# Performance work log

Hardware: AMD Instinct MI355X
Metric: run time of the kernel (lower is better)

Reference implementation:

```python
import jax, jax.numpy as jnp
import numpy as np
import math

B, NPG, DEG = 100, 500, 12          # graphs, nodes/graph, avg degree
F_IN, H, C = 128, 128, 10
RATIO = 0.5
N = B * NPG
E = N * DEG
K1 = math.ceil(NPG * RATIO)          # 250
K2 = math.ceil(K1 * RATIO)           # 125
K3 = math.ceil(K2 * RATIO)           # 63


def _lin(k, i, o):
    return jax.random.uniform(k, (i, o), jnp.float32, -1.0, 1.0) / np.sqrt(i).astype(np.float32)


def setup_inputs() -> dict:
    key = jax.random.key(0)
    ks = jax.random.split(key, 16)
    x = jax.random.normal(ks[0], (N, F_IN), jnp.float32)
    off = (jnp.arange(B, dtype=jnp.int32) * NPG)[:, None]
    src = (jax.random.randint(ks[1], (B, NPG * DEG), 0, NPG, jnp.int32) + off).reshape(-1)
    dst = (jax.random.randint(ks[2], (B, NPG * DEG), 0, NPG, jnp.int32) + off).reshape(-1)
    edge_index = jnp.stack([src, dst])
    return {
        'x': x, 'edge_index': edge_index,
        'Wl1': _lin(ks[3], F_IN, H), 'bl1': jnp.zeros((H,), jnp.float32), 'Wr1': _lin(ks[4], F_IN, H),
        'Wl2': _lin(ks[5], H, H), 'bl2': jnp.zeros((H,), jnp.float32), 'Wr2': _lin(ks[6], H, H),
        'Wl3': _lin(ks[7], H, H), 'bl3': jnp.zeros((H,), jnp.float32), 'Wr3': _lin(ks[8], H, H),
        'pw1': jax.random.normal(ks[9], (H,), jnp.float32),
        'pw2': jax.random.normal(ks[10], (H,), jnp.float32),
        'pw3': jax.random.normal(ks[11], (H,), jnp.float32),
        'W1': _lin(ks[12], 2 * H, H), 'b1': jnp.zeros((H,), jnp.float32),
        'W2': _lin(ks[13], H, H // 2), 'b2': jnp.zeros((H // 2,), jnp.float32),
        'W3': _lin(ks[14], H // 2, C), 'b3': jnp.zeros((C,), jnp.float32),
    }


def sage_conv(x, src, dst, emask, Wl, bl, Wr, n_nodes):
    # PyG SAGEConv: out_i = lin_l(mean_{j->i} x_j) + lin_r(x_i)
    msg = x[src] * emask[:, None]                                   # [E, d]
    agg = jax.ops.segment_sum(msg, dst, num_segments=n_nodes)
    cnt = jax.ops.segment_sum(emask, dst, num_segments=n_nodes)
    mean = agg / jnp.maximum(cnt, 1.0)[:, None]
    return mean @ Wl + bl + x @ Wr


def topk_pool(x, w, src, dst, emask, n_per, k):
    # TopKPooling: score = tanh(x.w/||w||); keep top-k nodes per graph; x_kept *= score
    score = jnp.tanh((x @ w) / jnp.linalg.norm(w))                  # [B*n_per]
    topv, topi = jax.lax.top_k(score.reshape(B, n_per), k)          # [B, k]
    perm = (topi + (jnp.arange(B, dtype=jnp.int32) * n_per)[:, None]).reshape(-1)
    x_new = x[perm] * topv.reshape(-1)[:, None]                     # [B*k, d]
    mapping = jnp.full((B * n_per,), -1, jnp.int32).at[perm].set(jnp.arange(B * k, dtype=jnp.int32))
    ns, nd = mapping[src], mapping[dst]
    emask_new = emask * ((ns >= 0) & (nd >= 0)).astype(emask.dtype)
    return x_new, jnp.maximum(ns, 0), jnp.maximum(nd, 0), emask_new


def readout(x, k):
    # global_max_pool || global_mean_pool (all graphs have exactly k nodes)
    xr = x.reshape(B, k, H)
    return jnp.concatenate([xr.max(axis=1), xr.mean(axis=1)], axis=1)  # [B, 2H]


def reference(x, edge_index, Wl1, bl1, Wr1, Wl2, bl2, Wr2, Wl3, bl3, Wr3,
              pw1, pw2, pw3, W1, b1, W2, b2, W3, b3):
    src, dst = edge_index[0], edge_index[1]
    emask = jnp.ones((E,), jnp.float32)
    h = jax.nn.relu(sage_conv(x, src, dst, emask, Wl1, bl1, Wr1, N))
    h, src, dst, emask = topk_pool(h, pw1, src, dst, emask, NPG, K1)
    x1 = readout(h, K1)
    h = jax.nn.relu(sage_conv(h, src, dst, emask, Wl2, bl2, Wr2, B * K1))
    h, src, dst, emask = topk_pool(h, pw2, src, dst, emask, K1, K2)
    x2 = readout(h, K2)
    h = jax.nn.relu(sage_conv(h, src, dst, emask, Wl3, bl3, Wr3, B * K2))
    h, src, dst, emask = topk_pool(h, pw3, src, dst, emask, K2, K3)
    x3 = readout(h, K3)
    z = x1 + x2 + x3
    z = jax.nn.relu(z @ W1 + b1)   # dropout is identity in eval mode
    z = jax.nn.relu(z @ W2 + b2)
    return jax.nn.log_softmax(z @ W3 + b3, axis=1)   # pool_loss == 0 for TopKPool
```

## Files before the change

### kernel.cpp

```cpp
#include <hip/hip_runtime.h>
#include <math.h>

#define BG    100
#define NPG   500
#define FD    128
#define EE    600000
#define EPG   6000
#define NN    50000
#define K1    250
#define K2    125
#define K3    63
#define CAP   64

typedef short v8s __attribute__((ext_vector_type(8)));
typedef float v4f __attribute__((ext_vector_type(4)));

__device__ __forceinline__ int swz(int p, int N) {
    int j = p & 7, i = p >> 3;
    int chunk = N >> 3, rem = N & 7;
    int mj = j < rem ? j : rem;
    return j * chunk + mj + i;
}

__device__ __forceinline__ unsigned short f2bf(float f) {
    unsigned int u = __float_as_uint(f);
    unsigned int r = (u + 0x7FFFu + ((u >> 16) & 1u)) >> 16;
    return (unsigned short)r;
}
__device__ __forceinline__ float bf2f(unsigned short b) {
    return __uint_as_float(((unsigned int)b) << 16);
}

__global__ __launch_bounds__(1024) void prep_fill_kernel(
        const int* __restrict__ ei, int* __restrict__ deg, int* __restrict__ col,
        const float* __restrict__ Wl1, const float* __restrict__ Wr1,
        const float* __restrict__ Wl2, const float* __restrict__ Wr2,
        const float* __restrict__ Wl3, const float* __restrict__ Wr3,
        unsigned short* __restrict__ wt_hi, unsigned short* __restrict__ wt_lo) {
    __shared__ int lcnt[NPG];
    int tid = threadIdx.x;
    if (blockIdx.x < BG) {
        int b = swz(blockIdx.x, BG);
        for (int i = tid; i < NPG; i += 1024) lcnt[i] = 0;
        __syncthreads();
        for (int e0 = tid; e0 < EPG; e0 += 1024) {
            int e = b * EPG + e0;
            int d = ei[EE + e];
            int pos = atomicAdd(&lcnt[d - b * NPG], 1);
            if (pos < CAP) col[(long long)d * CAP + pos] = ei[e];
        }
        __syncthreads();
        for (int i = tid; i < NPG; i += 1024) deg[b * NPG + i] = lcnt[i];
    } else {
        int id = (blockIdx.x - BG) * 1024 + tid;
        if (id >= 3 * 256 * 128) return;
        int layer = id >> 15, rem = id & 32767;
        int k = rem >> 7, n = rem & 127;
        const float* Wl = layer == 0 ? Wl1 : (layer == 1 ? Wl2 : Wl3);
        const float* Wr = layer == 0 ? Wr1 : (layer == 1 ? Wr2 : Wr3);
        float w = (k < 128) ? Wl[k * 128 + n] : Wr[(k - 128) * 128 + n];
        unsigned short hi = f2bf(w);
        unsigned short lo = f2bf(w - bf2f(hi));
        long long o = (long long)layer * 32768 + n * 256 + k;
        wt_hi[o] = hi;
        wt_lo[o] = lo;
    }
}

__global__ void gather_agg_kernel(const int* __restrict__ deg, const int* __restrict__ col,
                                  const float* __restrict__ x, float* __restrict__ mean,
                                  int n, int NB) {
    int g = swz(blockIdx.x, NB) * 256 + threadIdx.x;
    int node = g >> 5, sub = g & 31;
    if (node >= n) return;
    int d = deg[node]; if (d > CAP) d = CAP;
    const int* cp = col + (long long)node * CAP;
    float ax = 0.0f, ay = 0.0f, az = 0.0f, aw = 0.0f;
    int j = 0;
    for (; j + 4 <= d; j += 4) {
        int s0 = cp[j], s1 = cp[j + 1], s2 = cp[j + 2], s3 = cp[j + 3];
        float4 v0 = ((const float4*)(x + (long long)s0 * FD))[sub];
        float4 v1 = ((const float4*)(x + (long long)s1 * FD))[sub];
        float4 v2 = ((const float4*)(x + (long long)s2 * FD))[sub];
        float4 v3 = ((const float4*)(x + (long long)s3 * FD))[sub];
        ax += v0.x; ay += v0.y; az += v0.z; aw += v0.w;
        ax += v1.x; ay += v1.y; az += v1.z; aw += v1.w;
        ax += v2.x; ay += v2.y; az += v2.z; aw += v2.w;
        ax += v3.x; ay += v3.y; az += v3.z; aw += v3.w;
    }
    for (; j < d; ++j) {
        float4 v = ((const float4*)(x + (long long)cp[j] * FD))[sub];
        ax += v.x; ay += v.y; az += v.z; aw += v.w;
    }
    float inv = 1.0f / fmaxf((float)d, 1.0f);
    float4 o; o.x = ax * inv; o.y = ay * inv; o.z = az * inv; o.w = aw * inv;
    ((float4*)(mean + (long long)node * FD))[sub] = o;
}

__global__ __launch_bounds__(256) void sage_gemm_mfma_kernel(
        const float* __restrict__ mean, const float* __restrict__ x,
        const unsigned short* __restrict__ wt_hi, const unsigned short* __restrict__ wt_lo,
        const float* __restrict__ bl, const float* __restrict__ pw,
        float* __restrict__ hout, float* __restrict__ score, int M, int NB) {
    __shared__ unsigned short Bh[128 * 40], Bl[128 * 40];
    __shared__ float spart[64 * 16];
    __shared__ float snrmp[16];
    int tid  = threadIdx.x;
    int wave = tid >> 6, lane = tid & 63;
    int quad = lane >> 4, l15 = lane & 15;
    int row0 = swz(blockIdx.x, NB) * 64;

    v4f acc[8];
#pragma unroll
    for (int t = 0; t < 8; t++) acc[t] = (v4f){0.f, 0.f, 0.f, 0.f};

    if (tid < 16) {
        float s = 0.f;
#pragma unroll
        for (int t = 0; t < 8; t++) { float p = pw[t * 16 + tid]; s += p * p; }
        snrmp[tid] = s;
    }

    int growA = row0 + 16 * wave + l15; if (growA > M - 1) growA = M - 1;
    int brow = tid >> 1;
    int bk   = (tid & 1) * 16;

    for (int kt = 0; kt < 8; ++kt) {
        const float* Ab = (kt < 4) ? mean : x;
        const float* ap = Ab + (long long)growA * FD + ((kt < 4) ? kt : kt - 4) * 32 + quad * 8;
        float4 v0 = *(const float4*)(ap);
        float4 v1 = *(const float4*)(ap + 4);
        {
            int klog = kt * 32;
            const uint4* sh = (const uint4*)(wt_hi + (long long)brow * 256 + klog + bk);
            const uint4* sl = (const uint4*)(wt_lo + (long long)brow * 256 + klog + bk);
            uint4 vh0 = sh[0], vh1 = sh[1];
            uint4 vl0 = sl[0], vl1 = sl[1];
            *(uint4*)&Bh[brow * 40 + bk]     = vh0;
            *(uint4*)&Bh[brow * 40 + bk + 8] = vh1;
            *(uint4*)&Bl[brow * 40 + bk]     = vl0;
            *(uint4*)&Bl[brow * 40 + bk + 8] = vl1;
        }
        float f[8] = {v0.x, v0.y, v0.z, v0.w, v1.x, v1.y, v1.z, v1.w};
        v8s a_h, a_l;
#pragma unroll
        for (int q = 0; q < 8; q++) {
            unsigned short hb = f2bf(f[q]);
            a_h[q] = (short)hb;
            a_l[q] = (short)f2bf(f[q] - bf2f(hb));
        }
        __syncthreads();
#pragma unroll
        for (int t = 0; t < 8; t++) {
            v8s b_h = *(const v8s*)&Bh[(t * 16 + l15) * 40 + quad * 8];
            v8s b_l = *(const v8s*)&Bl[(t * 16 + l15) * 40 + quad * 8];
            acc[t] = __builtin_amdgcn_mfma_f32_16x16x32_bf16(a_l, b_h, acc[t], 0, 0, 0);
            acc[t] = __builtin_amdgcn_mfma_f32_16x16x32_bf16(a_h, b_l, acc[t], 0, 0, 0);
            acc[t] = __builtin_amdgcn_mfma_f32_16x16x32_bf16(a_h, b_h, acc[t], 0, 0, 0);
        }
        __syncthreads();
    }

    int rbase = row0 + 16 * wave + quad * 4;
    float part[4] = {0.f, 0.f, 0.f, 0.f};
#pragma unroll
    for (int t = 0; t < 8; t++) {
        int colc = t * 16 + l15;
        float blv = bl[colc];
        float pwv = pw[colc];
#pragma unroll
        for (int reg = 0; reg < 4; reg++) {
            float h = fmaxf(acc[t][reg] + blv, 0.0f);
            part[reg] += h * pwv;
            int grow = rbase + reg;
            if (grow < M) hout[(long long)grow * FD + colc] = h;
        }
    }
#pragma unroll
    for (int reg = 0; reg < 4; reg++)
        spart[(16 * wave + quad * 4 + reg) * 16 + l15] = part[reg];
    __syncthreads();
    if (tid < 64) {
        int grow = row0 + tid;
        if (grow < M) {
            float dot = 0.0f;
#pragma unroll
            for (int i = 0; i < 16; i++) dot += spart[tid * 16 + i];
            float nr = 0.0f;
#pragma unroll
            for (int i = 0; i < 16; i++) nr += snrmp[i];
            score[grow] = tanhf(dot / sqrtf(nr));
        }
    }
}

__global__ __launch_bounds__(1024) void topk_tail_kernel(
        const float* __restrict__ score, const float* __restrict__ hout,
        int n_per, int k, int SN,
        float* __restrict__ xp,
        const int* __restrict__ esrc, const int* __restrict__ edst,
        const float* __restrict__ em_in,
        int* __restrict__ src_out, int* __restrict__ dst_out, float* __restrict__ em_out,
        int* __restrict__ next_deg, int* __restrict__ next_col,
        float* __restrict__ z, int mode,
        const float* __restrict__ W1, const float* __restrict__ b1,
        const float* __restrict__ W2, const float* __restrict__ b2,
        const float* __restrict__ W3, const float* __restrict__ b3,
        float* __restrict__ out) {
    __shared__ float skey[512];
    __shared__ int   sidx[512];
    __shared__ int   lmap[512];
    __shared__ int   lcnt[512];
    __shared__ float pmax[1024];
    __shared__ float psum[1024];
    __shared__ float zs[256], t1[128], t2[64], t3[16];
    int b = swz(blockIdx.x, BG), tid = threadIdx.x;

    for (int i = tid; i < SN; i += 1024) {
        if (i < n_per) { skey[i] = score[b * n_per + i]; sidx[i] = i; }
        else           { skey[i] = -INFINITY;            sidx[i] = 0x7fffffff; }
        lmap[i] = -1;
        lcnt[i] = 0;
    }
    __syncthreads();

    for (int ks = 2; ks <= SN; ks <<= 1) {
        for (int j = ks >> 1; j > 0; j >>= 1) {
            for (int i = tid; i < SN; i += 1024) {
                int l = i ^ j;
                if (l > i) {
                    float ki = skey[i], kl = skey[l];
                    int   ii = sidx[i], il = sidx[l];
                    bool before = (ki > kl) || (ki == kl && ii < il);
                    bool up = ((i & ks) == 0);
                    if (up ? !before : before) {
                        skey[i] = kl; skey[l] = ki;
                        sidx[i] = il; sidx[l] = ii;
                    }
                }
            }
            __syncthreads();
        }
    }

    for (int i = tid; i < k; i += 1024) lmap[sidx[i]] = i;
    __syncthreads();

    if (esrc) {
        int nbase = b * n_per, kbase = b * k;
        for (int e0 = tid; e0 < EPG; e0 += 1024) {
            int e = b * EPG + e0;
            bool alive = em_in ? (em_in[e] != 0.0f) : true;
            if (alive) {
                int ls = lmap[esrc[e] - nbase];
                int ld = lmap[edst[e] - nbase];
                bool keep = (ls >= 0) && (ld >= 0);
                if (keep) {
                    int pos = atomicAdd(&lcnt[ld], 1);
                    if (pos < CAP) next_col[(long long)(kbase + ld) * CAP + pos] = kbase + ls;
                }
                if (em_out) {
                    em_out[e]  = keep ? 1.0f : 0.0f;
                    src_out[e] = keep ? kbase + ls : 0;
                    dst_out[e] = keep ? kbase + ld : 0;
                }
            } else if (em_out) {
                em_out[e] = 0.0f; src_out[e] = 0; dst_out[e] = 0;
            }
        }
        __syncthreads();
        for (int i = tid; i < k; i += 1024) next_deg[b * k + i] = lcnt[i];
    }

    int c = tid & 127, s = tid >> 7;
    float mx = -INFINITY, sm = 0.0f;
    {
        int r = s;
        long long hbase = (long long)b * n_per * FD + c;
        long long xbase = (long long)b * k * FD + c;
        for (; r + 24 < k; r += 32) {
            int i0 = sidx[r], i1 = sidx[r + 8], i2 = sidx[r + 16], i3 = sidx[r + 24];
            float k0 = skey[r], k1 = skey[r + 8], k2 = skey[r + 16], k3 = skey[r + 24];
            float v0 = hout[hbase + (long long)i0 * FD] * k0;
            float v1 = hout[hbase + (long long)i1 * FD] * k1;
            float v2 = hout[hbase + (long long)i2 * FD] * k2;
            float v3 = hout[hbase + (long long)i3 * FD] * k3;
            xp[xbase + (long long)(r)      * FD] = v0;
            xp[xbase + (long long)(r + 8)  * FD] = v1;
            xp[xbase + (long long)(r + 16) * FD] = v2;
            xp[xbase + (long long)(r + 24) * FD] = v3;
            mx = fmaxf(mx, v0); sm += v0;
            mx = fmaxf(mx, v1); sm += v1;
            mx = fmaxf(mx, v2); sm += v2;
            mx = fmaxf(mx, v3); sm += v3;
        }
        for (; r < k; r += 8) {
            float v = hout[hbase + (long long)sidx[r] * FD] * skey[r];
            xp[xbase + (long long)r * FD] = v;
            mx = fmaxf(mx, v); sm += v;
        }
    }
    pmax[tid] = mx; psum[tid] = sm;
    __syncthreads();
    if (tid < 128) {
        float m = -INFINITY, su = 0.0f;
#pragma unroll
        for (int i = 0; i < 8; i++) {
            m = fmaxf(m, pmax[i * 128 + tid]);
            su += psum[i * 128 + tid];
        }
        float mean = su / (float)k;
        if (mode == 0)      { z[b * 256 + tid] = m;  z[b * 256 + 128 + tid] = mean;  }
        else if (mode == 1) { z[b * 256 + tid] += m; z[b * 256 + 128 + tid] += mean; }
        else {
            zs[tid]       = z[b * 256 + tid] + m;
            zs[128 + tid] = z[b * 256 + 128 + tid] + mean;
        }
    }
    if (mode == 2) {
        __syncthreads();
        if (tid < 128) {
            float a = b1[tid];
            for (int kk = 0; kk < 256; kk++) a += zs[kk] * W1[kk * 128 + tid];
            t1[tid] = fmaxf(a, 0.0f);
        }
        __syncthreads();
        if (tid < 64) {
            float a = b2[tid];
            for (int kk = 0; kk < 128; kk++) a += t1[kk] * W2[kk * 64 + tid];
            t2[tid] = fmaxf(a, 0.0f);
        }
        __syncthreads();
        if (tid < 10) {
            float a = b3[tid];
            for (int kk = 0; kk < 64; kk++) a += t2[kk] * W3[kk * 10 + tid];
            t3[tid] = a;
        }
        __syncthreads();
        if (tid == 0) {
            float m = -INFINITY;
            for (int i = 0; i < 10; i++) m = fmaxf(m, t3[i]);
            float su = 0.0f;
            for (int i = 0; i < 10; i++) su += expf(t3[i] - m);
            float ls = logf(su);
            for (int i = 0; i < 10; i++) out[b * 10 + i] = t3[i] - m - ls;
        }
    }
}

extern "C" void kernel_launch(void* const* d_in, const int* in_sizes, int n_in,
                              void* d_out, int out_size, void* d_ws, size_t ws_size,
                              hipStream_t stream) {
    (void)in_sizes; (void)n_in; (void)out_size; (void)ws_size;
    const float* x   = (const float*)d_in[0];
    const int*   ei  = (const int*)d_in[1];
    const float* Wl1 = (const float*)d_in[2];
    const float* bl1 = (const float*)d_in[3];
    const float* Wr1 = (const float*)d_in[4];
    const float* Wl2 = (const float*)d_in[5];
    const float* bl2 = (const float*)d_in[6];
    const float* Wr2 = (const float*)d_in[7];
    const float* Wl3 = (const float*)d_in[8];
    const float* bl3 = (const float*)d_in[9];
    const float* Wr3 = (const float*)d_in[10];
    const float* pw1 = (const float*)d_in[11];
    const float* pw2 = (const float*)d_in[12];
    const float* pw3 = (const float*)d_in[13];
    const float* W1  = (const float*)d_in[14];
    const float* b1  = (const float*)d_in[15];
    const float* W2  = (const float*)d_in[16];
    const float* b2  = (const float*)d_in[17];
    const float* W3  = (const float*)d_in[18];
    const float* b3  = (const float*)d_in[19];
    float* out = (float*)d_out;

    char* ws = (char*)d_ws;
    size_t off = 0;
    auto alloc = [&](size_t bytes) {
        char* p = ws + off;
        off = (off + bytes + 255) & ~(size_t)255;
        return p;
    };
    float* mean  = (float*)alloc((size_t)NN * FD * 4);
    float* hout  = (float*)alloc((size_t)NN * FD * 4);
    float* xp    = (float*)alloc((size_t)BG * K1 * FD * 4);
    float* sc    = (float*)alloc((size_t)NN * 4);
    int*   srcb  = (int*)  alloc((size_t)EE * 4);
    int*   dstb  = (int*)  alloc((size_t)EE * 4);
    float* emb   = (float*)alloc((size_t)EE * 4);
    int*   deg   = (int*)  alloc((size_t)NN * 4);
    int*   colb  = (int*)  alloc((size_t)NN * CAP * 4);
    float* z     = (float*)alloc((size_t)BG * 256 * 4);
    unsigned short* wt_hi = (unsigned short*)alloc((size_t)3 * 32768 * 2);
    unsigned short* wt_lo = (unsigned short*)alloc((size_t)3 * 32768 * 2);

    prep_fill_kernel<<<BG + 96, 1024, 0, stream>>>(ei, deg, colb,
                                                   Wl1, Wr1, Wl2, Wr2, Wl3, Wr3, wt_hi, wt_lo);

    {
        int nb = (NN * 32 + 255) / 256;
        gather_agg_kernel<<<nb, 256, 0, stream>>>(deg, colb, x, mean, NN, nb);
    }
    {
        int nb = (NN + 63) / 64;
        sage_gemm_mfma_kernel<<<nb, 256, 0, stream>>>(mean, x, wt_hi, wt_lo,
                                                      bl1, pw1, hout, sc, NN, nb);
    }
    topk_tail_kernel<<<BG, 1024, 0, stream>>>(sc, hout, NPG, K1, 512, xp,
                                              ei, ei + EE, (const float*)0,
                                              srcb, dstb, emb, deg, colb,
                                              z, 0, W1, b1, W2, b2, W3, b3, out);

    const int N2 = BG * K1;
    {
        int nb = (N2 * 32 + 255) / 256;
        gather_agg_kernel<<<nb, 256, 0, stream>>>(deg, colb, xp, mean, N2, nb);
    }
    {
        int nb = (N2 + 63) / 64;
        sage_gemm_mfma_kernel<<<nb, 256, 0, stream>>>(mean, xp, wt_hi + 32768, wt_lo + 32768,
                                                      bl2, pw2, hout, sc, N2, nb);
    }
    topk_tail_kernel<<<BG, 1024, 0, stream>>>(sc, hout, K1, K2, 256, xp,
                                              srcb, dstb, emb,
                                              (int*)0, (int*)0, (float*)0, deg, colb,
                                              z, 1, W1, b1, W2, b2, W3, b3, out);

    const int N3 = BG * K2;
    {
        int nb = (N3 * 32 + 255) / 256;
        gather_agg_kernel<<<nb, 256, 0, stream>>>(deg, colb, xp, mean, N3, nb);
    }
    {
        int nb = (N3 + 63) / 64;
        sage_gemm_mfma_kernel<<<nb, 256, 0, stream>>>(mean, xp, wt_hi + 65536, wt_lo + 65536,
                                                      bl3, pw3, hout, sc, N3, nb);
    }
    topk_tail_kernel<<<BG, 1024, 0, stream>>>(sc, hout, K2, K3, 128, xp,
                                              (const int*)0, (const int*)0, (const float*)0,
                                              (int*)0, (int*)0, (float*)0, (int*)0, (int*)0,
                                              z, 2, W1, b1, W2, b2, W3, b3, out);
}
```

Before: 271.7 us.

## Fuse neighbor mean aggregation into SAGE GEMM and register-level bitonic top-k

Removes the separate gather_agg kernel and the mean buffer. Each GEMM thread now computes the neighbor mean for its A-fragment (its row and its 32 feature columns) in registers before the MFMA loop, which avoids writing and re-reading the mean tensor and saves three launches. Separately, the top-k bitonic sort packs score and index into a 64-bit key held in a register. It uses wave shuffles for strides under 64 and shared memory only for larger strides, cutting shared-memory traffic and barriers. The risk is the fused gather: each row's gather is split over only four lanes with 32 accumulator registers per thread, so memory-level parallelism may drop and register pressure may reduce occupancy.

After: 287.4 us. 5.8% more time.

```diff
diff --git a/kernel.cpp b/kernel.cpp
--- a/kernel.cpp
+++ b/kernel.cpp
@@ -67,38 +67,9 @@
     }
 }
 
-__global__ void gather_agg_kernel(const int* __restrict__ deg, const int* __restrict__ col,
-                                  const float* __restrict__ x, float* __restrict__ mean,
-                                  int n, int NB) {
-    int g = swz(blockIdx.x, NB) * 256 + threadIdx.x;
-    int node = g >> 5, sub = g & 31;
-    if (node >= n) return;
-    int d = deg[node]; if (d > CAP) d = CAP;
-    const int* cp = col + (long long)node * CAP;
-    float ax = 0.0f, ay = 0.0f, az = 0.0f, aw = 0.0f;
-    int j = 0;
-    for (; j + 4 <= d; j += 4) {
-        int s0 = cp[j], s1 = cp[j + 1], s2 = cp[j + 2], s3 = cp[j + 3];
-        float4 v0 = ((const float4*)(x + (long long)s0 * FD))[sub];
-        float4 v1 = ((const float4*)(x + (long long)s1 * FD))[sub];
-        float4 v2 = ((const float4*)(x + (long long)s2 * FD))[sub];
-        float4 v3 = ((const float4*)(x + (long long)s3 * FD))[sub];
-        ax += v0.x; ay += v0.y; az += v0.z; aw += v0.w;
-        ax += v1.x; ay += v1.y; az += v1.z; aw += v1.w;
-        ax += v2.x; ay += v2.y; az += v2.z; aw += v2.w;
-        ax += v3.x; ay += v3.y; az += v3.z; aw += v3.w;
-    }
-    for (; j < d; ++j) {
-        float4 v = ((const float4*)(x + (long long)cp[j] * FD))[sub];
-        ax += v.x; ay += v.y; az += v.z; aw += v.w;
-    }
-    float inv = 1.0f / fmaxf((float)d, 1.0f);
-    float4 o; o.x = ax * inv; o.y = ay * inv; o.z = az * inv; o.w = aw * inv;
-    ((float4*)(mean + (long long)node * FD))[sub] = o;
-}
-
-__global__ __launch_bounds__(256) void sage_gemm_mfma_kernel(
-        const float* __restrict__ mean, const float* __restrict__ x,
+__global__ __launch_bounds__(256) void sage_gemm_fused_kernel(
+        const int* __restrict__ deg, const int* __restrict__ col,
+        const float* __restrict__ x,
         const unsigned short* __restrict__ wt_hi, const unsigned short* __restrict__ wt_lo,
         const float* __restrict__ bl, const float* __restrict__ pw,
         float* __restrict__ hout, float* __restrict__ score, int M, int NB) {
@@ -125,11 +96,62 @@
     int brow = tid >> 1;
     int bk   = (tid & 1) * 16;
 
+    float macc[32];
+#pragma unroll
+    for (int q = 0; q < 32; q++) macc[q] = 0.0f;
+    {
+        int d = deg[growA]; if (d > CAP) d = CAP;
+        const int* cp = col + (long long)growA * CAP;
+        int j = 0;
+        for (; j + 2 <= d; j += 2) {
+            const float* r0 = x + (long long)cp[j]     * FD + quad * 8;
+            const float* r1 = x + (long long)cp[j + 1] * FD + quad * 8;
+#pragma unroll
+            for (int kt = 0; kt < 4; kt++) {
+                float4 a0 = *(const float4*)(r0 + kt * 32);
+                float4 a1 = *(const float4*)(r0 + kt * 32 + 4);
+                float4 c0 = *(const float4*)(r1 + kt * 32);
+                float4 c1 = *(const float4*)(r1 + kt * 32 + 4);
+                macc[kt * 8 + 0] += a0.x; macc[kt * 8 + 1] += a0.y;
+                macc[kt * 8 + 2] += a0.z; macc[kt * 8 + 3] += a0.w;
+                macc[kt * 8 + 4] += a1.x; macc[kt * 8 + 5] += a1.y;
+                macc[kt * 8 + 6] += a1.z; macc[kt * 8 + 7] += a1.w;
+                macc[kt * 8 + 0] += c0.x; macc[kt * 8 + 1] += c0.y;
+                macc[kt * 8 + 2] += c0.z; macc[kt * 8 + 3] += c0.w;
+                macc[kt * 8 + 4] += c1.x; macc[kt * 8 + 5] += c1.y;
+                macc[kt * 8 + 6] += c1.z; macc[kt * 8 + 7] += c1.w;
+            }
+        }
+        if (j < d) {
+            const float* r0 = x + (long long)cp[j] * FD + quad * 8;
+#pragma unroll
+            for (int kt = 0; kt < 4; kt++) {
+                float4 a0 = *(const float4*)(r0 + kt * 32);
+                float4 a1 = *(const float4*)(r0 + kt * 32 + 4);
+                macc[kt * 8 + 0] += a0.x; macc[kt * 8 + 1] += a0.y;
+                macc[kt * 8 + 2] += a0.z; macc[kt * 8 + 3] += a0.w;
+                macc[kt * 8 + 4] += a1.x; macc[kt * 8 + 5] += a1.y;
+                macc[kt * 8 + 6] += a1.z; macc[kt * 8 + 7] += a1.w;
+            }
+        }
+        float inv = 1.0f / fmaxf((float)d, 1.0f);
+#pragma unroll
+        for (int q = 0; q < 32; q++) macc[q] *= inv;
+    }
+
+#pragma unroll
     for (int kt = 0; kt < 8; ++kt) {
-        const float* Ab = (kt < 4) ? mean : x;
-        const float* ap = Ab + (long long)growA * FD + ((kt < 4) ? kt : kt - 4) * 32 + quad * 8;
-        float4 v0 = *(const float4*)(ap);
-        float4 v1 = *(const float4*)(ap + 4);
+        float f[8];
+        if (kt < 4) {
+#pragma unroll
+            for (int q = 0; q < 8; q++) f[q] = macc[kt * 8 + q];
+        } else {
+            const float* ap = x + (long long)growA * FD + (kt - 4) * 32 + quad * 8;
+            float4 v0 = *(const float4*)(ap);
+            float4 v1 = *(const float4*)(ap + 4);
+            f[0] = v0.x; f[1] = v0.y; f[2] = v0.z; f[3] = v0.w;
+            f[4] = v1.x; f[5] = v1.y; f[6] = v1.z; f[7] = v1.w;
+        }
         {
             int klog = kt * 32;
             const uint4* sh = (const uint4*)(wt_hi + (long long)brow * 256 + klog + bk);
@@ -141,7 +163,6 @@
             *(uint4*)&Bl[brow * 40 + bk]     = vl0;
             *(uint4*)&Bl[brow * 40 + bk + 8] = vl1;
         }
-        float f[8] = {v0.x, v0.y, v0.z, v0.w, v1.x, v1.y, v1.z, v1.w};
         v8s a_h, a_l;
 #pragma unroll
         for (int q = 0; q < 8; q++) {
@@ -209,6 +230,7 @@
         float* __restrict__ out) {
     __shared__ float skey[512];
     __shared__ int   sidx[512];
+    __shared__ unsigned long long spk[512];
     __shared__ int   lmap[512];
     __shared__ int   lcnt[512];
     __shared__ float pmax[1024];
@@ -216,34 +238,43 @@
     __shared__ float zs[256], t1[128], t2[64], t3[16];
     int b = swz(blockIdx.x, BG), tid = threadIdx.x;
 
-    for (int i = tid; i < SN; i += 1024) {
-        if (i < n_per) { skey[i] = score[b * n_per + i]; sidx[i] = i; }
-        else           { skey[i] = -INFINITY;            sidx[i] = 0x7fffffff; }
-        lmap[i] = -1;
-        lcnt[i] = 0;
-    }
-    __syncthreads();
+    for (int i = tid; i < SN; i += 1024) { lmap[i] = -1; lcnt[i] = 0; }
+
+    unsigned long long P = 0ULL;
+    if (tid < SN) {
+        float keyv; unsigned int idx;
+        if (tid < n_per) { keyv = score[b * n_per + tid]; idx = (unsigned int)tid; }
+        else             { keyv = -INFINITY;              idx = 0x7fffffffu; }
+        unsigned int u = __float_as_uint(keyv);
+        u = (u & 0x80000000u) ? ~u : (u | 0x80000000u);
+        P = ((unsigned long long)u << 32) | (unsigned long long)(~idx);
+    }
 
     for (int ks = 2; ks <= SN; ks <<= 1) {
         for (int j = ks >> 1; j > 0; j >>= 1) {
-            for (int i = tid; i < SN; i += 1024) {
-                int l = i ^ j;
-                if (l > i) {
-                    float ki = skey[i], kl = skey[l];
-                    int   ii = sidx[i], il = sidx[l];
-                    bool before = (ki > kl) || (ki == kl && ii < il);
-                    bool up = ((i & ks) == 0);
-                    if (up ? !before : before) {
-                        skey[i] = kl; skey[l] = ki;
-                        sidx[i] = il; sidx[l] = ii;
-                    }
-                }
+            unsigned long long Q;
+            if (j >= 64) {
+                __syncthreads();
+                if (tid < SN) spk[tid] = P;
+                __syncthreads();
+                Q = (tid < SN) ? spk[tid ^ j] : 0ULL;
+            } else {
+                Q = __shfl_xor(P, j, 64);
             }
-            __syncthreads();
-        }
-    }
-
-    for (int i = tid; i < k; i += 1024) lmap[sidx[i]] = i;
+            if (tid < SN) {
+                bool keepmax = (((tid & ks) == 0) == ((tid & j) == 0));
+                if (keepmax == (Q > P)) P = Q;
+            }
+        }
+    }
+    if (tid < SN) {
+        unsigned int u  = (unsigned int)(P >> 32);
+        unsigned int fb = (u & 0x80000000u) ? (u & 0x7fffffffu) : ~u;
+        int iv = (int)(~(unsigned int)P);
+        skey[tid] = __uint_as_float(fb);
+        sidx[tid] = iv;
+        if (tid < k) lmap[iv] = tid;
+    }
     __syncthreads();
 
     if (esrc) {
@@ -381,7 +412,6 @@
         off = (off + bytes + 255) & ~(size_t)255;
         return p;
     };
-    float* mean  = (float*)alloc((size_t)NN * FD * 4);
     float* hout  = (float*)alloc((size_t)NN * FD * 4);
     float* xp    = (float*)alloc((size_t)BG * K1 * FD * 4);
     float* sc    = (float*)alloc((size_t)NN * 4);
@@ -398,13 +428,9 @@
                                                    Wl1, Wr1, Wl2, Wr2, Wl3, Wr3, wt_hi, wt_lo);
 
     {
-        int nb = (NN * 32 + 255) / 256;
-        gather_agg_kernel<<<nb, 256, 0, stream>>>(deg, colb, x, mean, NN, nb);
-    }
-    {
         int nb = (NN + 63) / 64;
-        sage_gemm_mfma_kernel<<<nb, 256, 0, stream>>>(mean, x, wt_hi, wt_lo,
-                                                      bl1, pw1, hout, sc, NN, nb);
+        sage_gemm_fused_kernel<<<nb, 256, 0, stream>>>(deg, colb, x, wt_hi, wt_lo,
+                                                       bl1, pw1, hout, sc, NN, nb);
     }
     topk_tail_kernel<<<BG, 1024, 0, stream>>>(sc, hout, NPG, K1, 512, xp,
                                               ei, ei + EE, (const float*)0,
@@ -413,13 +439,9 @@
 
     const int N2 = BG * K1;
     {
-        int nb = (N2 * 32 + 255) / 256;
-        gather_agg_kernel<<<nb, 256, 0, stream>>>(deg, colb, xp, mean, N2, nb);
-    }
-    {
         int nb = (N2 + 63) / 64;
-        sage_gemm_mfma_kernel<<<nb, 256, 0, stream>>>(mean, xp, wt_hi + 32768, wt_lo + 32768,
-                                                      bl2, pw2, hout, sc, N2, nb);
+        sage_gemm_fused_kernel<<<nb, 256, 0, stream>>>(deg, colb, xp, wt_hi + 32768, wt_lo + 32768,
+                                                       bl2, pw2, hout, sc, N2, nb);
     }
     topk_tail_kernel<<<BG, 1024, 0, stream>>>(sc, hout, K1, K2, 256, xp,
                                               srcb, dstb, emb,
@@ -428,13 +450,9 @@
 
     const int N3 = BG * K2;
     {
-        int nb = (N3 * 32 + 255) / 256;
-        gather_agg_kernel<<<nb, 256, 0, stream>>>(deg, colb, xp, mean, N3, nb);
-    }
-    {
         int nb = (N3 + 63) / 64;
-        sage_gemm_mfma_kernel<<<nb, 256, 0, stream>>>(mean, xp, wt_hi + 65536, wt_lo + 65536,
-                                                      bl3, pw3, hout, sc, N3, nb);
+        sage_gemm_fused_kernel<<<nb, 256, 0, stream>>>(deg, colb, xp, wt_hi + 65536, wt_lo + 65536,
+                                                       bl3, pw3, hout, sc, N3, nb);
     }
     topk_tail_kernel<<<BG, 1024, 0, stream>>>(sc, hout, K2, K3, 128, xp,
                                               (const int*)0, (const int*)0, (const float*)0,
```
